# Performance work log

Hardware: AMD Instinct MI355X
Metric: run time of the kernel (lower is better)

## Reference

```python
import jax, jax.numpy as jnp
import numpy as np

N_NODES = 50000
N_EDGES = 1600000
IN_CH = 128
HID = 128  # 2 * out_channels
NUM_GRAPHS = 64


def gcn_conv(x, row, col, ew, W, b, num_nodes):
    # PyG GCNConv: add self-loops (weight 1), symmetric degree norm, x @ W,
    # gather at source row, scale by norm, scatter-add at target col, add bias.
    loop = jnp.arange(num_nodes)
    r = jnp.concatenate([row, loop])
    c = jnp.concatenate([col, loop])
    w = jnp.concatenate([ew, jnp.ones((num_nodes,), ew.dtype)])
    deg = jax.ops.segment_sum(w, c, num_segments=num_nodes)
    dis = jnp.where(deg > 0, jax.lax.rsqrt(jnp.where(deg > 0, deg, 1.0)), 0.0)
    norm = dis[r] * w * dis[c]  # [E+N]
    xw = x @ W  # [N, HID]
    msg = xw[r] * norm[:, None]  # [E+N, HID] gather + scale
    out = jax.ops.segment_sum(msg, c, num_segments=num_nodes)
    return out + b


def setup_inputs() -> dict:
    key = jax.random.key(0)
    ks = jax.random.split(key, 8)
    x = jax.random.normal(ks[0], (N_NODES, IN_CH), dtype=jnp.float32)
    edge_index = jax.random.randint(ks[1], (2, N_EDGES), 0, N_NODES, dtype=jnp.int64)
    edge_weight = jax.random.uniform(ks[2], (N_EDGES,), dtype=jnp.float32)
    batch = jnp.sort(jax.random.randint(ks[3], (N_NODES,), 0, NUM_GRAPHS, dtype=jnp.int64))
    W1 = jax.random.normal(ks[4], (IN_CH, HID), dtype=jnp.float32) * 0.01
    b1 = jnp.zeros((HID,), jnp.float32)
    W2 = jax.random.normal(ks[5], (HID, HID), dtype=jnp.float32) * 0.01
    b2 = jnp.zeros((HID,), jnp.float32)
    return {"x": x, "edge_index": edge_index, "edge_weight": edge_weight,
            "batch": batch, "W1": W1, "b1": b1, "W2": W2, "b2": b2}


def reference(x, edge_index, edge_weight, batch, W1, b1, W2, b2):
    row, col = edge_index[0], edge_index[1]
    h = jax.nn.relu(gcn_conv(x, row, col, edge_weight, W1, b1, N_NODES))
    h = jax.nn.relu(gcn_conv(h, row, col, edge_weight, W2, b2, N_NODES))
    # global_mean_pool over batch segment ids
    sums = jax.ops.segment_sum(h, batch, num_segments=NUM_GRAPHS)
    cnts = jax.ops.segment_sum(jnp.ones((N_NODES,), h.dtype), batch, num_segments=NUM_GRAPHS)
    pooled = sums / jnp.maximum(cnts, 1.0)[:, None]
    return h, pooled
```

## Files before the change

kernel.cpp:

```cpp
#include <hip/hip_runtime.h>


#define CH 128
#define BSH 7
#define NBLK 256
#define MAXNB 512
#define PCH 32

static __device__ __forceinline__ unsigned short f2bf(float f) {
    unsigned u = __float_as_uint(f);
    unsigned r = (u + 0x7FFF + ((u >> 16) & 1)) >> 16;
    return (unsigned short)r;
}

__global__ __launch_bounds__(256) void k_sort1a(const int* __restrict__ col,
                                                int* __restrict__ H, int E, int NB, int chunk) {
    __shared__ int hist[MAXNB];
    int t = threadIdx.x, blk = blockIdx.x;
    for (int i = t; i < NB; i += 256) hist[i] = 0;
    __syncthreads();
    int s = blk * chunk, e1 = min(s + chunk, E);
    for (int e = s + t; e < e1; e += 256) atomicAdd(&hist[col[e] >> BSH], 1);
    __syncthreads();
    for (int i = t; i < NB; i += 256) H[(size_t)i * NBLK + blk] = hist[i];
}

__global__ __launch_bounds__(1024) void k_scan1(int* __restrict__ data,
                                                int* __restrict__ bsum, int n) {
    __shared__ int sd[1024];
    int t = threadIdx.x;
    int i = blockIdx.x * 1024 + t;
    int v = (i < n) ? data[i] : 0;
    sd[t] = v;
    __syncthreads();
    for (int off = 1; off < 1024; off <<= 1) {
        int u = (t >= off) ? sd[t - off] : 0;
        __syncthreads();
        sd[t] += u;
        __syncthreads();
    }
    if (i < n) data[i] = sd[t] - v;
    if (t == 1023) bsum[blockIdx.x] = sd[1023];
}

__global__ __launch_bounds__(64) void k_scan2(int* bsum, int nb, int* total) {
    int t = threadIdx.x;
    if (nb <= 64) {
        int v = (t < nb) ? bsum[t] : 0;
        int orig = v;
        for (int off = 1; off < 64; off <<= 1) {
            int u = __shfl_up(v, off);
            if (t >= off) v += u;
        }
        if (t < nb) bsum[t] = v - orig;
        if (t == nb - 1) *total = v;
    } else if (t == 0) {
        int run = 0;
        for (int i = 0; i < nb; ++i) { int c = bsum[i]; bsum[i] = run; run += c; }
        *total = run;
    }
}

__global__ void k_scan3(int* data, const int* __restrict__ bsum, int n) {
    int i = blockIdx.x * 256 + threadIdx.x;
    if (i < n) data[i] += bsum[i >> 10];
}

__global__ __launch_bounds__(256) void k_sort1b(const int* __restrict__ row,
                                                const int* __restrict__ col,
                                                const float* __restrict__ ew,
                                                const int* __restrict__ Hs,
                                                int* __restrict__ cbuf,
                                                int2* __restrict__ pairs2,
                                                int E, int NB, int chunk) {
    __shared__ int cur[MAXNB];
    int t = threadIdx.x, blk = blockIdx.x;
    for (int i = t; i < NB; i += 256) cur[i] = Hs[(size_t)i * NBLK + blk];
    __syncthreads();
    int s = blk * chunk, e1 = min(s + chunk, E);
    for (int e = s + t; e < e1; e += 256) {
        int c = col[e];
        int pos = atomicAdd(&cur[c >> BSH], 1);
        cbuf[pos] = c;
        pairs2[pos] = make_int2(row[e], __float_as_int(ew[e]));
    }
}

__global__ __launch_bounds__(256) void k_sort2(const int* __restrict__ Hs,
                                               const int* __restrict__ cbuf,
                                               const int2* __restrict__ pairs2,
                                               int2* __restrict__ pairs,
                                               int* __restrict__ rowptr,
                                               float* __restrict__ dis,
                                               int E, int N, int NB) {
    __shared__ int hist[128];
    __shared__ int pref[128];
    __shared__ float wsum[128];
    int b = blockIdx.x, t = threadIdx.x;
    int n0 = b << BSH;
    int s = Hs[(size_t)b * NBLK];
    int e1 = (b + 1 < NB) ? Hs[(size_t)(b + 1) * NBLK] : E;
    if (t < 128) { hist[t] = 0; wsum[t] = 0.f; }
    __syncthreads();
    for (int e = s + t; e < e1; e += 256) atomicAdd(&hist[cbuf[e] - n0], 1);
    __syncthreads();
    if (t < 128) pref[t] = hist[t];
    __syncthreads();
    for (int off = 1; off < 128; off <<= 1) {
        int v = 0;
        if (t < 128 && t >= off) v = pref[t - off];
        __syncthreads();
        if (t < 128) pref[t] += v;
        __syncthreads();
    }
    if (t < 128) {
        int excl = pref[t] - hist[t];
        int node = n0 + t;
        if (node < N) rowptr[node] = s + excl;
        hist[t] = s + excl;
    }
    if (b == NB - 1 && t == 0) rowptr[N] = E;
    __syncthreads();
    for (int e = s + t; e < e1; e += 256) {
        int li = cbuf[e] - n0;
        int2 pr = pairs2[e];
        int pos = atomicAdd(&hist[li], 1);
        pairs[pos] = pr;
        atomicAdd(&wsum[li], __int_as_float(pr.y));
    }
    __syncthreads();
    if (t < 128 && n0 + t < N) dis[n0 + t] = rsqrtf(1.0f + wsum[t]);
}

__global__ __launch_bounds__(64) void k_norm(const int* __restrict__ rowptr,
                                             int2* __restrict__ pairs,
                                             const float* __restrict__ dis, int N) {
    int n = blockIdx.x;
    int lane = threadIdx.x;
    float dn = dis[n];
    int e0 = rowptr[n], e1 = rowptr[n + 1];
    for (int e = e0 + lane; e < e1; e += 64) {
        int2 p = pairs[e];
        float nn = dn * __int_as_float(p.y) * dis[p.x];
        pairs[e].y = __float_as_int(nn);
    }
}

__global__ __launch_bounds__(256) void k_gemm(const float* __restrict__ X,
                                              const float* __restrict__ W,
                                              unsigned short* __restrict__ Y, int N) {
    __shared__ float Ws[128][128];
    __shared__ float Xs[32][128];
    int tid = threadIdx.x;
    {
        const float4* Wv = (const float4*)W;
        float4* Sv = (float4*)&Ws[0][0];
#pragma unroll
        for (int i = 0; i < 16; ++i) Sv[tid + 256 * i] = Wv[tid + 256 * i];
    }
    int row0 = blockIdx.x * 32;
    {
        float4* Xsv = (float4*)&Xs[0][0];
        if (row0 + 32 <= N) {
            const float4* Xv = (const float4*)(X + (size_t)row0 * CH);
#pragma unroll
            for (int i = 0; i < 4; ++i) { int idx = tid + 256 * i; Xsv[idx] = Xv[idx]; }
        } else {
#pragma unroll
            for (int i = 0; i < 4; ++i) {
                int idx = tid + 256 * i;
                int r = idx >> 5;
                float4 v = make_float4(0.f, 0.f, 0.f, 0.f);
                if (row0 + r < N) v = ((const float4*)(X + (size_t)(row0 + r) * CH))[idx & 31];
                Xsv[idx] = v;
            }
        }
    }
    __syncthreads();
    int c4 = tid & 31;
    int rl = tid >> 5;
    float4 acc[4];
#pragma unroll
    for (int j = 0; j < 4; ++j) acc[j] = make_float4(0.f, 0.f, 0.f, 0.f);
    for (int k = 0; k < 128; k += 4) {
        float4 w0 = *(const float4*)&Ws[k + 0][c4 * 4];
        float4 w1 = *(const float4*)&Ws[k + 1][c4 * 4];
        float4 w2 = *(const float4*)&Ws[k + 2][c4 * 4];
        float4 w3 = *(const float4*)&Ws[k + 3][c4 * 4];
#pragma unroll
        for (int j = 0; j < 4; ++j) {
            float4 xv = *(const float4*)&Xs[rl + 8 * j][k];
            acc[j].x += xv.x * w0.x + xv.y * w1.x + xv.z * w2.x + xv.w * w3.x;
            acc[j].y += xv.x * w0.y + xv.y * w1.y + xv.z * w2.y + xv.w * w3.y;
            acc[j].z += xv.x * w0.z + xv.y * w1.z + xv.z * w2.z + xv.w * w3.z;
            acc[j].w += xv.x * w0.w + xv.y * w1.w + xv.z * w2.w + xv.w * w3.w;
        }
    }
#pragma unroll
    for (int j = 0; j < 4; ++j) {
        int r = row0 + rl + 8 * j;
        if (r < N) {
            ushort4 o;
            o.x = f2bf(acc[j].x); o.y = f2bf(acc[j].y);
            o.z = f2bf(acc[j].z); o.w = f2bf(acc[j].w);
            *(ushort4*)&Y[(size_t)r * CH + c4 * 4] = o;
        }
    }
}

__global__ __launch_bounds__(64) void k_agg(const unsigned int* __restrict__ XW,
                                            const float* __restrict__ dis,
                                            const int* __restrict__ rowptr,
                                            const int2* __restrict__ pairs,
                                            const float* __restrict__ bias,
                                            float* __restrict__ OUT, int N) {
    int n = blockIdx.x;
    if (n >= N) return;
    int lane = threadIdx.x;
    float d = dis[n];
    float sn = d * d;
    unsigned a = XW[(size_t)n * 64 + lane];
    float ax = __uint_as_float(a << 16) * sn;
    float ay = __uint_as_float(a & 0xFFFF0000u) * sn;
    int e0 = rowptr[n], e1 = rowptr[n + 1];
    int e = e0;
    for (; e + 4 <= e1; e += 4) {
        int2 p0 = pairs[e], p1 = pairs[e + 1], p2 = pairs[e + 2], p3 = pairs[e + 3];
        unsigned v0 = XW[(size_t)p0.x * 64 + lane];
        unsigned v1 = XW[(size_t)p1.x * 64 + lane];
        unsigned v2 = XW[(size_t)p2.x * 64 + lane];
        unsigned v3 = XW[(size_t)p3.x * 64 + lane];
        float n0 = __int_as_float(p0.y), n1 = __int_as_float(p1.y);
        float n2 = __int_as_float(p2.y), n3 = __int_as_float(p3.y);
        ax += n0 * __uint_as_float(v0 << 16) + n1 * __uint_as_float(v1 << 16)
            + n2 * __uint_as_float(v2 << 16) + n3 * __uint_as_float(v3 << 16);
        ay += n0 * __uint_as_float(v0 & 0xFFFF0000u) + n1 * __uint_as_float(v1 & 0xFFFF0000u)
            + n2 * __uint_as_float(v2 & 0xFFFF0000u) + n3 * __uint_as_float(v3 & 0xFFFF0000u);
    }
    for (; e < e1; ++e) {
        int2 p = pairs[e];
        unsigned v = XW[(size_t)p.x * 64 + lane];
        float nn = __int_as_float(p.y);
        ax += nn * __uint_as_float(v << 16);
        ay += nn * __uint_as_float(v & 0xFFFF0000u);
    }
    float2 b = ((const float2*)bias)[lane];
    ax = fmaxf(ax + b.x, 0.f);
    ay = fmaxf(ay + b.y, 0.f);
    ((float2*)OUT)[(size_t)n * 64 + lane] = make_float2(ax, ay);
}

__device__ __forceinline__ int lowerb(const int* a, int n, int v) {
    int lo = 0, hi = n;
    while (lo < hi) {
        int m = (lo + hi) >> 1;
        if (a[m] < v) lo = m + 1; else hi = m;
    }
    return lo;
}

__global__ __launch_bounds__(128) void k_pool1(const float* __restrict__ H,
                                               const int* __restrict__ batch,
                                               float* __restrict__ partial, int N) {
    __shared__ int ss[2];
    int g = blockIdx.x / PCH;
    int k = blockIdx.x % PCH;
    if (threadIdx.x == 0) {
        ss[0] = lowerb(batch, N, g);
        ss[1] = lowerb(batch, N, g + 1);
    }
    __syncthreads();
    int s = ss[0], len = ss[1] - ss[0];
    int cs = s + (int)(((long long)len * k) / PCH);
    int ce = s + (int)(((long long)len * (k + 1)) / PCH);
    int ch = threadIdx.x;
    float a0 = 0.f, a1 = 0.f;
    int n = cs;
    for (; n + 2 <= ce; n += 2) {
        a0 += H[(size_t)(n + 0) * CH + ch];
        a1 += H[(size_t)(n + 1) * CH + ch];
    }
    for (; n < ce; ++n) a0 += H[(size_t)n * CH + ch];
    partial[(size_t)blockIdx.x * CH + ch] = a0 + a1;
}

__global__ __launch_bounds__(128) void k_pool2(const float* __restrict__ partial,
                                               const int* __restrict__ batch,
                                               float* __restrict__ P, int N) {
    __shared__ int ss[2];
    int g = blockIdx.x;
    if (threadIdx.x == 0) {
        ss[0] = lowerb(batch, N, g);
        ss[1] = lowerb(batch, N, g + 1);
    }
    __syncthreads();
    int ch = threadIdx.x;
    float a = 0.f;
#pragma unroll
    for (int k = 0; k < PCH; ++k) a += partial[(size_t)(g * PCH + k) * CH + ch];
    float c = (float)(ss[1] - ss[0]);
    P[(size_t)g * CH + ch] = a / fmaxf(c, 1.f);
}

extern "C" void kernel_launch(void* const* d_in, const int* in_sizes, int n_in,
                              void* d_out, int out_size, void* d_ws, size_t ws_size,
                              hipStream_t stream) {
    const float* x     = (const float*)d_in[0];
    const int*   ei    = (const int*)d_in[1];
    const float* ew    = (const float*)d_in[2];
    const int*   batch = (const int*)d_in[3];
    const float* W1    = (const float*)d_in[4];
    const float* b1    = (const float*)d_in[5];
    const float* W2    = (const float*)d_in[6];
    const float* b2    = (const float*)d_in[7];

    int N = in_sizes[0] / CH;
    int E = in_sizes[1] / 2;
    const int* row = ei;
    const int* col = ei + E;

    float* out    = (float*)d_out;
    float* h      = out;
    float* pooled = out + (size_t)N * CH;

    int NB    = (N + 127) >> BSH;
    int chunk = (E + NBLK - 1) / NBLK;
    int n2    = NB * NBLK;

    char* wsb = (char*)d_ws;
    size_t oN  = ((size_t)N * 4 + 255) & ~(size_t)255;
    size_t oN1 = ((size_t)(N + 1) * 4 + 255) & ~(size_t)255;
    size_t oH  = ((size_t)(n2 + 1) * 4 + 255) & ~(size_t)255;
    size_t oB  = 512;
    size_t oE2 = ((size_t)E * 8 + 255) & ~(size_t)255;
    size_t oE1 = ((size_t)E * 4 + 255) & ~(size_t)255;
    float* dis    = (float*)wsb;
    int*   rowptr = (int*)(wsb + oN);
    int*   H      = (int*)(wsb + oN + oN1);
    int*   bsum   = (int*)(wsb + oN + oN1 + oH);
    int2*  pairs  = (int2*)(wsb + oN + oN1 + oH + oB);
    int*   cbuf   = (int*)(wsb + oN + oN1 + oH + oB + oE2);
    unsigned short* xw = (unsigned short*)(wsb + oN + oN1 + oH + oB + oE2 + oE1);
    int2*  pairs2 = (int2*)xw;
    float* partial = (float*)cbuf;

    int sb2 = (n2 + 1023) / 1024;

    k_sort1a<<<NBLK, 256, 0, stream>>>(col, H, E, NB, chunk);
    k_scan1<<<sb2, 1024, 0, stream>>>(H, bsum, n2);
    k_scan2<<<1, 64, 0, stream>>>(bsum, sb2, H + n2);
    k_scan3<<<(n2 + 255) / 256, 256, 0, stream>>>(H, bsum, n2);
    k_sort1b<<<NBLK, 256, 0, stream>>>(row, col, ew, H, cbuf, pairs2, E, NB, chunk);
    k_sort2<<<NB, 256, 0, stream>>>(H, cbuf, pairs2, pairs, rowptr, dis, E, N, NB);
    k_norm<<<N, 64, 0, stream>>>(rowptr, pairs, dis, N);

    int gb = (N + 31) / 32;
    k_gemm<<<gb, 256, 0, stream>>>(x, W1, xw, N);
    k_agg<<<N, 64, 0, stream>>>((const unsigned int*)xw, dis, rowptr, pairs, b1, h, N);
    k_gemm<<<gb, 256, 0, stream>>>(h, W2, xw, N);
    k_agg<<<N, 64, 0, stream>>>((const unsigned int*)xw, dis, rowptr, pairs, b2, h, N);
    k_pool1<<<64 * PCH, 128, 0, stream>>>(h, batch, partial, N);
    k_pool2<<<64, 128, 0, stream>>>(partial, batch, pooled, N);
}
```

Before: 274.7 us.

## Split aggregation into column chunks with packed fp16-norm edge indices

The GEMM output is stored column-chunked, as four slabs of 32 bf16 channels, so each aggregation pass gathers from a 3.2 MB slab that can stay in cache. Edge source index and normalisation are packed into one 32-bit word: a 17-bit index plus a 15-bit fp16 norm with the sign bit dropped. Each pass uses four edge groups of 16 lanes per node, combined with cross-lane shuffles. The edge list is now read four times per layer, and the norm loses precision by going to fp16.

```diff
diff --git a/kernel.cpp b/kernel.cpp
--- a/kernel.cpp
+++ b/kernel.cpp
@@ -1,4 +1,5 @@
 #include <hip/hip_runtime.h>
+#include <hip/hip_fp16.h>
 
 
 #define CH 128
@@ -6,11 +7,18 @@
 #define NBLK 256
 #define MAXNB 512
 #define PCH 32
+#define TCH 4
 
 static __device__ __forceinline__ unsigned short f2bf(float f) {
     unsigned u = __float_as_uint(f);
     unsigned r = (u + 0x7FFF + ((u >> 16) & 1)) >> 16;
     return (unsigned short)r;
+}
+static __device__ __forceinline__ float bflo(unsigned v) { return __uint_as_float(v << 16); }
+static __device__ __forceinline__ float bfhi(unsigned v) { return __uint_as_float(v & 0xFFFF0000u); }
+static __device__ __forceinline__ float f16u(unsigned p) {
+    __half_raw hr; hr.x = (unsigned short)(p & 0x7FFF);
+    return __half2float(*reinterpret_cast<__half*>(&hr));
 }
 
 __global__ __launch_bounds__(256) void k_sort1a(const int* __restrict__ col,
@@ -133,8 +141,9 @@
 }
 
 __global__ __launch_bounds__(64) void k_norm(const int* __restrict__ rowptr,
-                                             int2* __restrict__ pairs,
-                                             const float* __restrict__ dis, int N) {
+                                             const int2* __restrict__ pairs,
+                                             const float* __restrict__ dis,
+                                             unsigned* __restrict__ epk, int N) {
     int n = blockIdx.x;
     int lane = threadIdx.x;
     float dn = dis[n];
@@ -142,7 +151,9 @@
     for (int e = e0 + lane; e < e1; e += 64) {
         int2 p = pairs[e];
         float nn = dn * __int_as_float(p.y) * dis[p.x];
-        pairs[e].y = __float_as_int(nn);
+        __half hh = __float2half(nn);
+        unsigned short hb = *reinterpret_cast<unsigned short*>(&hh);
+        epk[e] = ((unsigned)p.x << 15) | (unsigned)(hb & 0x7FFF);
     }
 }
 
@@ -196,6 +207,8 @@
             acc[j].w += xv.x * w0.w + xv.y * w1.w + xv.z * w2.w + xv.w * w3.w;
         }
     }
+    int c  = c4 >> 3;
+    int of = (c4 & 7) * 4;
 #pragma unroll
     for (int j = 0; j < 4; ++j) {
         int r = row0 + rl + 8 * j;
@@ -203,51 +216,57 @@
             ushort4 o;
             o.x = f2bf(acc[j].x); o.y = f2bf(acc[j].y);
             o.z = f2bf(acc[j].z); o.w = f2bf(acc[j].w);
-            *(ushort4*)&Y[(size_t)r * CH + c4 * 4] = o;
+            *(ushort4*)&Y[(size_t)c * N * 32 + (size_t)r * 32 + of] = o;
         }
     }
 }
 
-__global__ __launch_bounds__(64) void k_agg(const unsigned int* __restrict__ XW,
-                                            const float* __restrict__ dis,
-                                            const int* __restrict__ rowptr,
-                                            const int2* __restrict__ pairs,
-                                            const float* __restrict__ bias,
-                                            float* __restrict__ OUT, int N) {
-    int n = blockIdx.x;
+__global__ __launch_bounds__(256) void k_aggc(const unsigned int* __restrict__ XWC,
+                                              const float* __restrict__ dis,
+                                              const int* __restrict__ rowptr,
+                                              const unsigned int* __restrict__ epk,
+                                              const float* __restrict__ bias,
+                                              float* __restrict__ OUT,
+                                              int col0, int N) {
+    int n = blockIdx.x * 4 + (threadIdx.x >> 6);
     if (n >= N) return;
-    int lane = threadIdx.x;
-    float d = dis[n];
-    float sn = d * d;
-    unsigned a = XW[(size_t)n * 64 + lane];
-    float ax = __uint_as_float(a << 16) * sn;
-    float ay = __uint_as_float(a & 0xFFFF0000u) * sn;
+    int lane = threadIdx.x & 63;
+    int g  = lane >> 4;
+    int li = lane & 15;
+    float ax = 0.f, ay = 0.f;
     int e0 = rowptr[n], e1 = rowptr[n + 1];
-    int e = e0;
-    for (; e + 4 <= e1; e += 4) {
-        int2 p0 = pairs[e], p1 = pairs[e + 1], p2 = pairs[e + 2], p3 = pairs[e + 3];
-        unsigned v0 = XW[(size_t)p0.x * 64 + lane];
-        unsigned v1 = XW[(size_t)p1.x * 64 + lane];
-        unsigned v2 = XW[(size_t)p2.x * 64 + lane];
-        unsigned v3 = XW[(size_t)p3.x * 64 + lane];
-        float n0 = __int_as_float(p0.y), n1 = __int_as_float(p1.y);
-        float n2 = __int_as_float(p2.y), n3 = __int_as_float(p3.y);
-        ax += n0 * __uint_as_float(v0 << 16) + n1 * __uint_as_float(v1 << 16)
-            + n2 * __uint_as_float(v2 << 16) + n3 * __uint_as_float(v3 << 16);
-        ay += n0 * __uint_as_float(v0 & 0xFFFF0000u) + n1 * __uint_as_float(v1 & 0xFFFF0000u)
-            + n2 * __uint_as_float(v2 & 0xFFFF0000u) + n3 * __uint_as_float(v3 & 0xFFFF0000u);
-    }
-    for (; e < e1; ++e) {
-        int2 p = pairs[e];
-        unsigned v = XW[(size_t)p.x * 64 + lane];
-        float nn = __int_as_float(p.y);
-        ax += nn * __uint_as_float(v << 16);
-        ay += nn * __uint_as_float(v & 0xFFFF0000u);
-    }
-    float2 b = ((const float2*)bias)[lane];
-    ax = fmaxf(ax + b.x, 0.f);
-    ay = fmaxf(ay + b.y, 0.f);
-    ((float2*)OUT)[(size_t)n * 64 + lane] = make_float2(ax, ay);
+    int e = e0 + g;
+    for (; e + 4 < e1; e += 8) {
+        unsigned p0 = __builtin_nontemporal_load(&epk[e]);
+        unsigned p1 = __builtin_nontemporal_load(&epk[e + 4]);
+        unsigned v0 = XWC[(size_t)(p0 >> 15) * 16 + li];
+        unsigned v1 = XWC[(size_t)(p1 >> 15) * 16 + li];
+        float n0 = f16u(p0), n1 = f16u(p1);
+        ax += n0 * bflo(v0) + n1 * bflo(v1);
+        ay += n0 * bfhi(v0) + n1 * bfhi(v1);
+    }
+    if (e < e1) {
+        unsigned p = __builtin_nontemporal_load(&epk[e]);
+        unsigned v = XWC[(size_t)(p >> 15) * 16 + li];
+        float nn = f16u(p);
+        ax += nn * bflo(v);
+        ay += nn * bfhi(v);
+    }
+    if (g == 0) {
+        float d = dis[n];
+        float sn = d * d;
+        unsigned a = XWC[(size_t)n * 16 + li];
+        ax += sn * bflo(a);
+        ay += sn * bfhi(a);
+    }
+    ax += __shfl_xor(ax, 16); ay += __shfl_xor(ay, 16);
+    ax += __shfl_xor(ax, 32); ay += __shfl_xor(ay, 32);
+    if (g == 0) {
+        float2 b = *(const float2*)&bias[col0 + li * 2];
+        ax = fmaxf(ax + b.x, 0.f);
+        ay = fmaxf(ay + b.y, 0.f);
+        *(float2*)&OUT[(size_t)n * CH + col0 + li * 2] = make_float2(ax, ay);
+    }
 }
 
 __device__ __forceinline__ int lowerb(const int* a, int n, int v) {
@@ -342,6 +361,7 @@
     int*   cbuf   = (int*)(wsb + oN + oN1 + oH + oB + oE2);
     unsigned short* xw = (unsigned short*)(wsb + oN + oN1 + oH + oB + oE2 + oE1);
     int2*  pairs2 = (int2*)xw;
+    unsigned* epk = (unsigned*)cbuf;
     float* partial = (float*)cbuf;
 
     int sb2 = (n2 + 1023) / 1024;
@@ -352,13 +372,18 @@
     k_scan3<<<(n2 + 255) / 256, 256, 0, stream>>>(H, bsum, n2);
     k_sort1b<<<NBLK, 256, 0, stream>>>(row, col, ew, H, cbuf, pairs2, E, NB, chunk);
     k_sort2<<<NB, 256, 0, stream>>>(H, cbuf, pairs2, pairs, rowptr, dis, E, N, NB);
-    k_norm<<<N, 64, 0, stream>>>(rowptr, pairs, dis, N);
+    k_norm<<<N, 64, 0, stream>>>(rowptr, pairs, dis, epk, N);
 
     int gb = (N + 31) / 32;
+    int ab = (N + 3) / 4;
     k_gemm<<<gb, 256, 0, stream>>>(x, W1, xw, N);
-    k_agg<<<N, 64, 0, stream>>>((const unsigned int*)xw, dis, rowptr, pairs, b1, h, N);
+    for (int c = 0; c < TCH; ++c)
+        k_aggc<<<ab, 256, 0, stream>>>((const unsigned int*)(xw + (size_t)c * N * 32),
+                                       dis, rowptr, epk, b1, h, c * 32, N);
     k_gemm<<<gb, 256, 0, stream>>>(h, W2, xw, N);
-    k_agg<<<N, 64, 0, stream>>>((const unsigned int*)xw, dis, rowptr, pairs, b2, h, N);
+    for (int c = 0; c < TCH; ++c)
+        k_aggc<<<ab, 256, 0, stream>>>((const unsigned int*)(xw + (size_t)c * N * 32),
+                                       dis, rowptr, epk, b2, h, c * 32, N);
     k_pool1<<<64 * PCH, 128, 0, stream>>>(h, batch, partial, N);
     k_pool2<<<64, 128, 0, stream>>>(partial, batch, pooled, N);
 }
```

Measured after the change: 473.5 us. 72.4% more time.

## Pack local column index into row bits and raise sort block count

Applied to the files above, without the earlier changes.

Removes the separate cbuf array by packing the 7-bit local target index into the upper bits of the source row index inside the pairs2 entries. This drops one 4-byte write and two 4-byte reads per edge in the bucket sort. The number of histogram blocks also rises from 256 to 1024 to give the two sort passes more parallelism, and scan2 becomes a 1024-thread shared-memory scan to cope with the larger block-sum array. The packing assumes node ids fit in 17 bits (N=50000 does), and the pool partials now reuse the H buffer.

```diff
diff --git a/kernel.cpp b/kernel.cpp
--- a/kernel.cpp
+++ b/kernel.cpp
@@ -3,7 +3,7 @@
 
 #define CH 128
 #define BSH 7
-#define NBLK 256
+#define NBLK 1024
 #define MAXNB 512
 #define PCH 32
 
@@ -43,22 +43,20 @@
     if (t == 1023) bsum[blockIdx.x] = sd[1023];
 }
 
-__global__ __launch_bounds__(64) void k_scan2(int* bsum, int nb, int* total) {
+__global__ __launch_bounds__(1024) void k_scan2(int* bsum, int nb, int* total) {
+    __shared__ int sd[1024];
     int t = threadIdx.x;
-    if (nb <= 64) {
-        int v = (t < nb) ? bsum[t] : 0;
-        int orig = v;
-        for (int off = 1; off < 64; off <<= 1) {
-            int u = __shfl_up(v, off);
-            if (t >= off) v += u;
-        }
-        if (t < nb) bsum[t] = v - orig;
-        if (t == nb - 1) *total = v;
-    } else if (t == 0) {
-        int run = 0;
-        for (int i = 0; i < nb; ++i) { int c = bsum[i]; bsum[i] = run; run += c; }
-        *total = run;
-    }
+    int v = (t < nb) ? bsum[t] : 0;
+    sd[t] = v;
+    __syncthreads();
+    for (int off = 1; off < 1024; off <<= 1) {
+        int u = (t >= off) ? sd[t - off] : 0;
+        __syncthreads();
+        sd[t] += u;
+        __syncthreads();
+    }
+    if (t < nb) bsum[t] = sd[t] - v;
+    if (t == 1023) *total = sd[1023];
 }
 
 __global__ void k_scan3(int* data, const int* __restrict__ bsum, int n) {
@@ -70,7 +68,6 @@
                                                 const int* __restrict__ col,
                                                 const float* __restrict__ ew,
                                                 const int* __restrict__ Hs,
-                                                int* __restrict__ cbuf,
                                                 int2* __restrict__ pairs2,
                                                 int E, int NB, int chunk) {
     __shared__ int cur[MAXNB];
@@ -81,13 +78,11 @@
     for (int e = s + t; e < e1; e += 256) {
         int c = col[e];
         int pos = atomicAdd(&cur[c >> BSH], 1);
-        cbuf[pos] = c;
-        pairs2[pos] = make_int2(row[e], __float_as_int(ew[e]));
+        pairs2[pos] = make_int2(row[e] | ((c & 127) << 17), __float_as_int(ew[e]));
     }
 }
 
 __global__ __launch_bounds__(256) void k_sort2(const int* __restrict__ Hs,
-                                               const int* __restrict__ cbuf,
                                                const int2* __restrict__ pairs2,
                                                int2* __restrict__ pairs,
                                                int* __restrict__ rowptr,
@@ -102,7 +97,8 @@
     int e1 = (b + 1 < NB) ? Hs[(size_t)(b + 1) * NBLK] : E;
     if (t < 128) { hist[t] = 0; wsum[t] = 0.f; }
     __syncthreads();
-    for (int e = s + t; e < e1; e += 256) atomicAdd(&hist[cbuf[e] - n0], 1);
+    for (int e = s + t; e < e1; e += 256)
+        atomicAdd(&hist[(unsigned)pairs2[e].x >> 17], 1);
     __syncthreads();
     if (t < 128) pref[t] = hist[t];
     __syncthreads();
@@ -122,10 +118,10 @@
     if (b == NB - 1 && t == 0) rowptr[N] = E;
     __syncthreads();
     for (int e = s + t; e < e1; e += 256) {
-        int li = cbuf[e] - n0;
         int2 pr = pairs2[e];
+        int li = (unsigned)pr.x >> 17;
         int pos = atomicAdd(&hist[li], 1);
-        pairs[pos] = pr;
+        pairs[pos] = make_int2(pr.x & 0x1FFFF, pr.y);
         atomicAdd(&wsum[li], __int_as_float(pr.y));
     }
     __syncthreads();
@@ -331,27 +327,25 @@
     size_t oN  = ((size_t)N * 4 + 255) & ~(size_t)255;
     size_t oN1 = ((size_t)(N + 1) * 4 + 255) & ~(size_t)255;
     size_t oH  = ((size_t)(n2 + 1) * 4 + 255) & ~(size_t)255;
-    size_t oB  = 512;
+    size_t oB  = 4096;
     size_t oE2 = ((size_t)E * 8 + 255) & ~(size_t)255;
-    size_t oE1 = ((size_t)E * 4 + 255) & ~(size_t)255;
     float* dis    = (float*)wsb;
     int*   rowptr = (int*)(wsb + oN);
     int*   H      = (int*)(wsb + oN + oN1);
     int*   bsum   = (int*)(wsb + oN + oN1 + oH);
     int2*  pairs  = (int2*)(wsb + oN + oN1 + oH + oB);
-    int*   cbuf   = (int*)(wsb + oN + oN1 + oH + oB + oE2);
-    unsigned short* xw = (unsigned short*)(wsb + oN + oN1 + oH + oB + oE2 + oE1);
+    unsigned short* xw = (unsigned short*)(wsb + oN + oN1 + oH + oB + oE2);
     int2*  pairs2 = (int2*)xw;
-    float* partial = (float*)cbuf;
+    float* partial = (float*)H;
 
     int sb2 = (n2 + 1023) / 1024;
 
     k_sort1a<<<NBLK, 256, 0, stream>>>(col, H, E, NB, chunk);
     k_scan1<<<sb2, 1024, 0, stream>>>(H, bsum, n2);
-    k_scan2<<<1, 64, 0, stream>>>(bsum, sb2, H + n2);
+    k_scan2<<<1, 1024, 0, stream>>>(bsum, sb2, H + n2);
     k_scan3<<<(n2 + 255) / 256, 256, 0, stream>>>(H, bsum, n2);
-    k_sort1b<<<NBLK, 256, 0, stream>>>(row, col, ew, H, cbuf, pairs2, E, NB, chunk);
-    k_sort2<<<NB, 256, 0, stream>>>(H, cbuf, pairs2, pairs, rowptr, dis, E, N, NB);
+    k_sort1b<<<NBLK, 256, 0, stream>>>(row, col, ew, H, pairs2, E, NB, chunk);
+    k_sort2<<<NB, 256, 0, stream>>>(H, pairs2, pairs, rowptr, dis, E, N, NB);
     k_norm<<<N, 64, 0, stream>>>(rowptr, pairs, dis, N);
 
     int gb = (N + 31) / 32;
```

Measured after the change: 261.3 us. 1.05x faster.
